# Kernel tuning notes

Hardware: AMD Instinct MI355X
Metric: run time of the kernel (lower is better)

Reference implementation:

```python
import jax, jax.numpy as jnp
import numpy as np
from jax import lax

G = 8  # number of RBF grid points (FastKAN default style)
GRID = jnp.linspace(-2.0, 2.0, G)
DENOM = 4.0 / (G - 1)  # grid spacing used as gaussian width


def _fastkan_conv(x, ln_w, ln_b, Wb, bb, Ws):
    # x: [B, C, H, W]; 3x3 conv, stride 1, pad 1 via patch unfold + FastKAN linear
    B, C, H, W = x.shape
    p = lax.conv_general_dilated_patches(x, (3, 3), (1, 1), ((1, 1), (1, 1)))  # [B, C*9, H, W]
    p = p.transpose(0, 2, 3, 1).reshape(B * H * W, C * 9)  # [N, in]
    # LayerNorm over patch features (FastKAN normalizes before the RBF basis)
    mu = p.mean(-1, keepdims=True)
    var = p.var(-1, keepdims=True)
    pn = (p - mu) / jnp.sqrt(var + 1e-5) * ln_w + ln_b
    # Gaussian RBF basis: [N, in, G]
    rbf = jnp.exp(-jnp.square((pn[:, :, None] - GRID) / DENOM))
    spline = rbf.reshape(B * H * W, -1) @ Ws.T          # [N, out]
    base = jax.nn.silu(p) @ Wb.T + bb                    # [N, out]
    out = spline + base
    return out.reshape(B, H, W, -1).transpose(0, 3, 1, 2)  # [B, out, H, W]


def _bn_relu_pool(h, gamma, beta):
    # BatchNorm2d in training mode (batch stats), ReLU, MaxPool2d(2,2)
    mu = h.mean((0, 2, 3), keepdims=True)
    var = h.var((0, 2, 3), keepdims=True)
    h = (h - mu) / jnp.sqrt(var + 1e-5) * gamma[None, :, None, None] + beta[None, :, None, None]
    h = jax.nn.relu(h)
    return lax.reduce_window(h, -jnp.inf, lax.max, (1, 1, 2, 2), (1, 1, 2, 2), 'VALID')


def setup_inputs() -> dict:
    key = jax.random.key(0)
    ks = jax.random.split(key, 16)
    B, Cin, H, W = 32, 16, 64, 64
    dims = [(Cin * 9, 64), (64 * 9, 128), (128 * 9, 256)]
    inp = {"x": jax.random.normal(ks[0], (B, Cin, H, W), jnp.float32)}
    for i, (fin, fout) in enumerate(dims, 1):
        inp[f"ln_w{i}"] = jnp.ones((fin,), jnp.float32)
        inp[f"ln_b{i}"] = jnp.zeros((fin,), jnp.float32)
        inp[f"Wb{i}"] = jax.random.normal(ks[3 * i], (fout, fin), jnp.float32) * 0.05
        inp[f"bb{i}"] = jnp.zeros((fout,), jnp.float32)
        inp[f"Ws{i}"] = jax.random.normal(ks[3 * i + 1], (fout, fin * G), jnp.float32) * 0.05
        inp[f"g{i}"] = jnp.ones((fout,), jnp.float32)
        inp[f"be{i}"] = jnp.zeros((fout,), jnp.float32)
    return inp


def reference(x, ln_w1, ln_b1, Wb1, bb1, Ws1, g1, be1,
              ln_w2, ln_b2, Wb2, bb2, Ws2, g2, be2,
              ln_w3, ln_b3, Wb3, bb3, Ws3, g3, be3):
    h = _bn_relu_pool(_fastkan_conv(x, ln_w1, ln_b1, Wb1, bb1, Ws1), g1, be1)
    h = _bn_relu_pool(_fastkan_conv(h, ln_w2, ln_b2, Wb2, bb2, Ws2), g2, be2)
    h = _bn_relu_pool(_fastkan_conv(h, ln_w3, ln_b3, Wb3, bb3, Ws3), g3, be3)
    return h.reshape(h.shape[0], -1)  # flatten: [B, 256*8*8]
```

## Files before the change

### kernel.cpp

```cpp
#include <hip/hip_runtime.h>

typedef _Float16 half_t;
typedef __attribute__((ext_vector_type(8))) _Float16 half8;
typedef __attribute__((ext_vector_type(4))) float floatx4;


#define RBF_SCALE 2.1019644f
#define RBF_G0   -4.2039288f
#define RBF_2D    2.40224482f
#define RBF_D2    1.44269504f
#define RBF_Q     0.13533528f

template<int C, int H, int W>
__global__ __launch_bounds__(256)
void ln_prep(const float* __restrict__ x,
             const float* __restrict__ lnw, const float* __restrict__ lnb,
             half_t* __restrict__ pn, half_t* __restrict__ sp)
{
    const int HW = H * W, IN = C * 9;
    const int NL = (IN + 63) / 64;
    const int wv = threadIdx.x >> 6, lane = threadIdx.x & 63;
    const int pix = blockIdx.x * 4 + wv;
    const int b = pix / HW, hw = pix % HW, h = hw / W, w = hw % W;
    const float* xb = x + (long)b * C * HW;

    float v[NL];
    float s = 0.f, s2 = 0.f;
    #pragma unroll
    for (int t = 0; t < NL; ++t) {
        int i = t * 64 + lane;
        float val = 0.f;
        if (i < IN) {
            int ch = i / 9, r = i - ch * 9;
            int y = h + r / 3 - 1, xx = w + r % 3 - 1;
            if (y >= 0 && y < H && xx >= 0 && xx < W)
                val = xb[ch * HW + y * W + xx];
        }
        v[t] = val; s += val; s2 += val * val;
    }
    #pragma unroll
    for (int off = 32; off > 0; off >>= 1) {
        s  += __shfl_down(s,  off, 64);
        s2 += __shfl_down(s2, off, 64);
    }
    s = __shfl(s, 0, 64); s2 = __shfl(s2, 0, 64);
    float mean = s / IN;
    float istd = rsqrtf(s2 / IN - mean * mean + 1e-5f);

    #pragma unroll
    for (int t = 0; t < NL; ++t) {
        int i = t * 64 + lane;
        if (i < IN) {
            float val = v[t];
            float pnv = (val - mean) * istd * lnw[i] + lnb[i];
            pnv = fminf(12.f, fmaxf(-12.f, pnv * RBF_SCALE));
            pn[(long)pix * IN + i] = (half_t)pnv;
            sp[(long)pix * IN + i] = (half_t)(val / (1.f + __expf(-val)));
        }
    }
}

template<int IN, int OUT>
__global__ __launch_bounds__(256)
void conv_w(const float* __restrict__ Ws, const float* __restrict__ Wb,
            half_t* __restrict__ Wt)
{
    const int NIB = (IN + 63) / 64, NSTEP = NIB * 9;
    int idx = blockIdx.x * 256 + threadIdx.x;
    if (idx >= OUT * NSTEP * 64) return;
    int uu = idx & 63;
    int t = idx >> 6;
    int o = t % OUT;
    int s = t / OUT;
    int iblk = s / 9, j = s % 9;
    int ulin = (((uu >> 3) ^ (o & 7)) << 3) + (uu & 7);
    int i = iblk * 64 + ulin;
    float v = 0.f;
    if (i < IN)
        v = (j < 8) ? Ws[(long)o * IN * 8 + i * 8 + j] : Wb[(long)o * IN + i];
    Wt[idx] = (half_t)v;
}

template<int IN, int OUT, int HW, int NB, int SPLIT>
__global__ __launch_bounds__(256)
void kan_gemm(const half_t* __restrict__ pn, const half_t* __restrict__ sp,
              const half_t* __restrict__ Wt, float* __restrict__ out)
{
    const int NIB = (IN + 63) / 64;

    __shared__ half_t As[2][64 * 64];
    __shared__ half_t Bs[2][NB * 64 * 64];

    const int tid = threadIdx.x;
    const int row = tid >> 2, q = tid & 3;
    const int pix = blockIdx.x * 64 + row;
    const half_t* pnrow = pn + (long)pix * IN;
    const half_t* sprow = sp + (long)pix * IN;

    const int wv = tid >> 6, lane = tid & 63;
    const int lr = lane & 15, lq = lane >> 4;
    const int u0 = (2 * q) ^ (row & 7);
    const int u1 = (2 * q + 1) ^ (row & 7);
    const int yoff = blockIdx.y * (4 * NB * 16);

    floatx4 acc[NB][4] = {};
    float r[16], u[16];

    const int grpA = (blockIdx.z * NIB) / SPLIT;
    const int grpB = ((blockIdx.z + 1) * NIB) / SPLIT;
    const int s0 = grpA * 9, s1 = grpB * 9;

    int jg = 0, ibg = grpA;

    auto stageB = [&](int it, int buf) {
        const half_t* wsrc = Wt + (long)it * OUT * 64
                              + (long)(yoff + wv * NB * 16) * 64;
        #pragma unroll
        for (int c = 0; c < NB * 2; ++c) {
            __builtin_amdgcn_global_load_lds(
                (const __attribute__((address_space(1))) void*)(wsrc + c * 512 + lane * 8),
                (__attribute__((address_space(3))) void*)(&Bs[buf][wv * NB * 1024 + c * 512]),
                16, 0, 0);
        }
    };

    auto genA = [&](int buf) {
        const int i0 = ibg * 64 + q * 16;
        const bool ok = (i0 < IN);
        if (jg < 8) {
            if (jg == 0) {
                const half_t* pp = pnrow + (ok ? i0 : 0);
                half8 p0 = *(const half8*)pp;
                half8 p1 = *(const half8*)(pp + 8);
                #pragma unroll
                for (int kk = 0; kk < 8; ++kk) {
                    float t0 = (float)p0[kk], t1 = (float)p1[kk];
                    float d0 = t0 - RBF_G0, d1 = t1 - RBF_G0;
                    r[kk]     = ok ? __builtin_amdgcn_exp2f(-(d0 * d0)) : 0.f;
                    u[kk]     = ok ? __builtin_amdgcn_exp2f(fmaf(RBF_2D, d0, -RBF_D2)) : 0.f;
                    r[kk + 8] = ok ? __builtin_amdgcn_exp2f(-(d1 * d1)) : 0.f;
                    u[kk + 8] = ok ? __builtin_amdgcn_exp2f(fmaf(RBF_2D, d1, -RBF_D2)) : 0.f;
                }
            }
            half8 a0, a1;
            #pragma unroll
            for (int kk = 0; kk < 8; ++kk) {
                a0[kk] = (half_t)r[kk];
                a1[kk] = (half_t)r[kk + 8];
            }
            *(half8*)&As[buf][row * 64 + u0 * 8] = a0;
            *(half8*)&As[buf][row * 64 + u1 * 8] = a1;
            if (jg < 7) {
                #pragma unroll
                for (int kk = 0; kk < 16; ++kk) { r[kk] *= u[kk]; u[kk] *= RBF_Q; }
            }
        } else {
            half8 a0 = half8{}, a1 = half8{};
            if (ok) {
                a0 = *(const half8*)(sprow + i0);
                a1 = *(const half8*)(sprow + i0 + 8);
            }
            *(half8*)&As[buf][row * 64 + u0 * 8] = a0;
            *(half8*)&As[buf][row * 64 + u1 * 8] = a1;
        }
        if (++jg == 9) { jg = 0; ++ibg; }
    };

    auto domfma = [&](int buf) {
        __builtin_amdgcn_s_setprio(1);
        #pragma unroll
        for (int ks = 0; ks < 2; ++ks) {
            half8 af[4], bf[NB];
            #pragma unroll
            for (int mf = 0; mf < 4; ++mf) {
                int rr = mf * 16 + lr;
                af[mf] = *(const half8*)&As[buf][rr * 64 + (((ks * 4 + lq) ^ (rr & 7)) * 8)];
            }
            #pragma unroll
            for (int nb = 0; nb < NB; ++nb) {
                int rr = wv * NB * 16 + nb * 16 + lr;
                bf[nb] = *(const half8*)&Bs[buf][rr * 64 + (((ks * 4 + lq) ^ (rr & 7)) * 8)];
            }
            #pragma unroll
            for (int nb = 0; nb < NB; ++nb)
                #pragma unroll
                for (int mf = 0; mf < 4; ++mf)
                    acc[nb][mf] = __builtin_amdgcn_mfma_f32_16x16x32_f16(
                        bf[nb], af[mf], acc[nb][mf], 0, 0, 0);
        }
        __builtin_amdgcn_s_setprio(0);
    };

    stageB(s0, 0);
    genA(0);
    __syncthreads();

    for (int it = s0; it < s1; ++it) {
        const int cur = (it - s0) & 1, nxt = cur ^ 1;
        if (it + 1 < s1) {
            stageB(it + 1, nxt);
            genA(nxt);
        }
        domfma(cur);
        __syncthreads();
    }

    const long zoff = (long)blockIdx.z * ((long)gridDim.x * 64) * OUT;
    #pragma unroll
    for (int nb = 0; nb < NB; ++nb)
    #pragma unroll
    for (int mf = 0; mf < 4; ++mf)
    #pragma unroll
    for (int reg = 0; reg < 4; ++reg) {
        int o  = yoff + wv * NB * 16 + nb * 16 + lq * 4 + reg;
        int p2 = blockIdx.x * 64 + mf * 16 + lr;
        int b2 = p2 / HW, hw2 = p2 % HW;
        out[zoff + ((long)b2 * OUT + o) * HW + hw2] = acc[nb][mf][reg];
    }
}

__launch_bounds__(256)
__global__ void bn_stats(const float* __restrict__ h, const float* __restrict__ bias,
                         int C, int HW, int B, int nz, float* __restrict__ sums)
{
    int c = blockIdx.y;
    float bbc = bias[c];
    long zstride = (long)B * C * HW;
    int total = B * HW;
    float s = 0.f, s2 = 0.f;
    for (int idx = blockIdx.x * 256 + threadIdx.x; idx < total; idx += 256 * gridDim.x) {
        int b = idx / HW, r = idx % HW;
        long base = ((long)b * C + c) * HW + r;
        float v = bbc;
        for (int z = 0; z < nz; ++z) v += h[z * zstride + base];
        s += v; s2 += v * v;
    }
    for (int off = 32; off > 0; off >>= 1) {
        s  += __shfl_down(s,  off, 64);
        s2 += __shfl_down(s2, off, 64);
    }
    __shared__ float rs[4], rs2[4];
    int lane = threadIdx.x & 63, wid = threadIdx.x >> 6;
    if (lane == 0) { rs[wid] = s; rs2[wid] = s2; }
    __syncthreads();
    if (threadIdx.x == 0) {
        atomicAdd(&sums[c],     rs[0] + rs[1] + rs[2] + rs[3]);
        atomicAdd(&sums[C + c], rs2[0] + rs2[1] + rs2[2] + rs2[3]);
    }
}

__launch_bounds__(256)
__global__ void bn_relu_pool(const float* __restrict__ h, const float* __restrict__ sums,
                             const float* __restrict__ bias,
                             const float* __restrict__ gamma, const float* __restrict__ beta,
                             float* __restrict__ out, int B, int C, int H, int W, int nz)
{
    int Ho = H / 2, Wo = W / 2;
    long total = (long)B * C * Ho * Wo;
    long idx = (long)blockIdx.x * 256 + threadIdx.x;
    if (idx >= total) return;
    int pw = idx % Wo; long t = idx / Wo;
    int ph = t % Ho; t /= Ho;
    int c = t % C; int b = (int)(t / C);

    float M = (float)B * H * W;
    float mean = sums[c] / M;
    float var  = sums[C + c] / M - mean * mean;
    float scale = gamma[c] * rsqrtf(var + 1e-5f);
    float shift = beta[c] - mean * scale + bias[c] * scale;

    long zstride = (long)B * C * H * W;
    const float* hp = h + ((long)b * C + c) * H * W;
    float m = 0.f;
    #pragma unroll
    for (int i = 0; i < 2; ++i)
        #pragma unroll
        for (int j = 0; j < 2; ++j) {
            long off = (2 * ph + i) * W + 2 * pw + j;
            float v = 0.f;
            for (int z = 0; z < nz; ++z) v += hp[z * zstride + off];
            v = v * scale + shift;
            m = fmaxf(m, v);
        }
    out[idx] = m;
}

extern "C" void kernel_launch(void* const* d_in, const int* in_sizes, int n_in,
                              void* d_out, int out_size, void* d_ws, size_t ws_size,
                              hipStream_t stream) {
    const float* x     = (const float*)d_in[0];
    const float* ln_w1 = (const float*)d_in[1];  const float* ln_b1 = (const float*)d_in[2];
    const float* Wb1   = (const float*)d_in[3];  const float* bb1   = (const float*)d_in[4];
    const float* Ws1   = (const float*)d_in[5];  const float* g1    = (const float*)d_in[6];
    const float* be1   = (const float*)d_in[7];
    const float* ln_w2 = (const float*)d_in[8];  const float* ln_b2 = (const float*)d_in[9];
    const float* Wb2   = (const float*)d_in[10]; const float* bb2   = (const float*)d_in[11];
    const float* Ws2   = (const float*)d_in[12]; const float* g2    = (const float*)d_in[13];
    const float* be2   = (const float*)d_in[14];
    const float* ln_w3 = (const float*)d_in[15]; const float* ln_b3 = (const float*)d_in[16];
    const float* Wb3   = (const float*)d_in[17]; const float* bb3   = (const float*)d_in[18];
    const float* Ws3   = (const float*)d_in[19]; const float* g3    = (const float*)d_in[20];
    const float* be3   = (const float*)d_in[21];

    const int B = 32;
    char* ws = (char*)d_ws;
    float*  convbuf = (float*)(ws + 0);
    float*  poolbuf = (float*)(ws + 33554432);
    float*  stats1  = (float*)(ws + 41943040);
    float*  stats2  = (float*)(ws + 41945088);
    float*  stats3  = (float*)(ws + 41947136);
    half_t* wt1     = (half_t*)(ws + 41949184);
    half_t* wt2     = (half_t*)(ws + 42170368);
    half_t* wt3     = (half_t*)(ws + 43497472);
    half_t* pnbuf   = (half_t*)(ws + 48805888);
    half_t* spbuf   = (half_t*)(ws + 86554624);

    hipMemsetAsync(stats1, 0, 6144, stream);

    conv_w<144, 64><<<(64 * 27 * 64 + 255) / 256, 256, 0, stream>>>(Ws1, Wb1, wt1);
    conv_w<576, 128><<<(128 * 81 * 64 + 255) / 256, 256, 0, stream>>>(Ws2, Wb2, wt2);
    conv_w<1152, 256><<<(256 * 162 * 64 + 255) / 256, 256, 0, stream>>>(Ws3, Wb3, wt3);

    {
        const int H = 64, W = 64, OUT = 64;
        int npix = B * H * W;
        ln_prep<16, H, W><<<npix / 4, 256, 0, stream>>>(x, ln_w1, ln_b1, pnbuf, spbuf);
        kan_gemm<144, OUT, H * W, 1, 1><<<dim3(npix / 64, 1, 1), 256, 0, stream>>>(
            pnbuf, spbuf, wt1, convbuf);
        bn_stats<<<dim3(64, OUT), 256, 0, stream>>>(convbuf, bb1, OUT, H * W, B, 1, stats1);
        long tot = (long)B * OUT * (H / 2) * (W / 2);
        bn_relu_pool<<<(tot + 255) / 256, 256, 0, stream>>>(
            convbuf, stats1, bb1, g1, be1, poolbuf, B, OUT, H, W, 1);
    }
    {
        const int H = 32, W = 32, OUT = 128;
        int npix = B * H * W;
        ln_prep<64, H, W><<<npix / 4, 256, 0, stream>>>(poolbuf, ln_w2, ln_b2, pnbuf, spbuf);
        kan_gemm<576, OUT, H * W, 2, 2><<<dim3(npix / 64, 1, 2), 256, 0, stream>>>(
            pnbuf, spbuf, wt2, convbuf);
        bn_stats<<<dim3(16, OUT), 256, 0, stream>>>(convbuf, bb2, OUT, H * W, B, 2, stats2);
        long tot = (long)B * OUT * (H / 2) * (W / 2);
        bn_relu_pool<<<(tot + 255) / 256, 256, 0, stream>>>(
            convbuf, stats2, bb2, g2, be2, poolbuf, B, OUT, H, W, 2);
    }
    {
        const int H = 16, W = 16, OUT = 256;
        int npix = B * H * W;
        ln_prep<128, H, W><<<npix / 4, 256, 0, stream>>>(poolbuf, ln_w3, ln_b3, pnbuf, spbuf);
        kan_gemm<1152, OUT, H * W, 2, 4><<<dim3(npix / 64, 2, 4), 256, 0, stream>>>(
            pnbuf, spbuf, wt3, convbuf);
        bn_stats<<<dim3(8, OUT), 256, 0, stream>>>(convbuf, bb3, OUT, H * W, B, 4, stats3);
        long tot = (long)B * OUT * (H / 2) * (W / 2);
        bn_relu_pool<<<(tot + 255) / 256, 256, 0, stream>>>(
            convbuf, stats3, bb3, g3, be3, (float*)d_out, B, OUT, H, W, 4);
    }
}
```

Baseline: 512.5 us.

## Single-buffer LDS tiles in KAN GEMM and prefetch A inputs into registers

Replaces the double-buffered A/B shared-memory tiles with single buffers and two barriers per k-step. This halves LDS use, which may allow more resident blocks per CU. The pn/sp row chunks are now prefetched into registers one stage ahead, and the out-of-range masking is dropped because zero-padded weights cancel those lanes. The cost is that the weight global-to-LDS load and the A generation are no longer overlapped with the MFMA work inside a block, so latency hiding now depends on other resident blocks.

```diff
diff --git a/kernel.cpp b/kernel.cpp
--- a/kernel.cpp
+++ b/kernel.cpp
@@ -88,8 +88,8 @@
 {
     const int NIB = (IN + 63) / 64;
 
-    __shared__ half_t As[2][64 * 64];
-    __shared__ half_t Bs[2][NB * 64 * 64];
+    __shared__ half_t As[64 * 64];
+    __shared__ half_t Bs[NB * 64 * 64];
 
     const int tid = threadIdx.x;
     const int row = tid >> 2, q = tid & 3;
@@ -105,6 +105,7 @@
 
     floatx4 acc[NB][4] = {};
     float r[16], u[16];
+    half8 pf0, pf1;
 
     const int grpA = (blockIdx.z * NIB) / SPLIT;
     const int grpB = ((blockIdx.z + 1) * NIB) / SPLIT;
@@ -112,34 +113,36 @@
 
     int jg = 0, ibg = grpA;
 
-    auto stageB = [&](int it, int buf) {
+    auto ldglob = [&](const half_t* base, int ib, half8& a, half8& b) {
+        int i0 = ib * 64 + q * 16;
+        const half_t* pp = base + ((i0 < IN) ? i0 : 0);
+        a = *(const half8*)pp;
+        b = *(const half8*)(pp + 8);
+    };
+
+    auto stageB = [&](int it) {
         const half_t* wsrc = Wt + (long)it * OUT * 64
                               + (long)(yoff + wv * NB * 16) * 64;
         #pragma unroll
         for (int c = 0; c < NB * 2; ++c) {
             __builtin_amdgcn_global_load_lds(
                 (const __attribute__((address_space(1))) void*)(wsrc + c * 512 + lane * 8),
-                (__attribute__((address_space(3))) void*)(&Bs[buf][wv * NB * 1024 + c * 512]),
+                (__attribute__((address_space(3))) void*)(&Bs[wv * NB * 1024 + c * 512]),
                 16, 0, 0);
         }
     };
 
-    auto genA = [&](int buf) {
-        const int i0 = ibg * 64 + q * 16;
-        const bool ok = (i0 < IN);
+    auto genA = [&]() {
         if (jg < 8) {
             if (jg == 0) {
-                const half_t* pp = pnrow + (ok ? i0 : 0);
-                half8 p0 = *(const half8*)pp;
-                half8 p1 = *(const half8*)(pp + 8);
                 #pragma unroll
                 for (int kk = 0; kk < 8; ++kk) {
-                    float t0 = (float)p0[kk], t1 = (float)p1[kk];
-                    float d0 = t0 - RBF_G0, d1 = t1 - RBF_G0;
-                    r[kk]     = ok ? __builtin_amdgcn_exp2f(-(d0 * d0)) : 0.f;
-                    u[kk]     = ok ? __builtin_amdgcn_exp2f(fmaf(RBF_2D, d0, -RBF_D2)) : 0.f;
-                    r[kk + 8] = ok ? __builtin_amdgcn_exp2f(-(d1 * d1)) : 0.f;
-                    u[kk + 8] = ok ? __builtin_amdgcn_exp2f(fmaf(RBF_2D, d1, -RBF_D2)) : 0.f;
+                    float d0 = (float)pf0[kk] - RBF_G0;
+                    float d1 = (float)pf1[kk] - RBF_G0;
+                    r[kk]     = __builtin_amdgcn_exp2f(-(d0 * d0));
+                    u[kk]     = __builtin_amdgcn_exp2f(fmaf(RBF_2D, d0, -RBF_D2));
+                    r[kk + 8] = __builtin_amdgcn_exp2f(-(d1 * d1));
+                    u[kk + 8] = __builtin_amdgcn_exp2f(fmaf(RBF_2D, d1, -RBF_D2));
                 }
             }
             half8 a0, a1;
@@ -148,25 +151,22 @@
                 a0[kk] = (half_t)r[kk];
                 a1[kk] = (half_t)r[kk + 8];
             }
-            *(half8*)&As[buf][row * 64 + u0 * 8] = a0;
-            *(half8*)&As[buf][row * 64 + u1 * 8] = a1;
+            *(half8*)&As[row * 64 + u0 * 8] = a0;
+            *(half8*)&As[row * 64 + u1 * 8] = a1;
             if (jg < 7) {
                 #pragma unroll
                 for (int kk = 0; kk < 16; ++kk) { r[kk] *= u[kk]; u[kk] *= RBF_Q; }
             }
+            if (jg == 7) ldglob(sprow, ibg, pf0, pf1);
         } else {
-            half8 a0 = half8{}, a1 = half8{};
-            if (ok) {
-                a0 = *(const half8*)(sprow + i0);
-                a1 = *(const half8*)(sprow + i0 + 8);
-            }
-            *(half8*)&As[buf][row * 64 + u0 * 8] = a0;
-            *(half8*)&As[buf][row * 64 + u1 * 8] = a1;
+            *(half8*)&As[row * 64 + u0 * 8] = pf0;
+            *(half8*)&As[row * 64 + u1 * 8] = pf1;
+            ldglob(pnrow, ibg + 1, pf0, pf1);
         }
         if (++jg == 9) { jg = 0; ++ibg; }
     };
 
-    auto domfma = [&](int buf) {
+    auto domfma = [&]() {
         __builtin_amdgcn_s_setprio(1);
         #pragma unroll
         for (int ks = 0; ks < 2; ++ks) {
@@ -174,12 +174,12 @@
             #pragma unroll
             for (int mf = 0; mf < 4; ++mf) {
                 int rr = mf * 16 + lr;
-                af[mf] = *(const half8*)&As[buf][rr * 64 + (((ks * 4 + lq) ^ (rr & 7)) * 8)];
+                af[mf] = *(const half8*)&As[rr * 64 + (((ks * 4 + lq) ^ (rr & 7)) * 8)];
             }
             #pragma unroll
             for (int nb = 0; nb < NB; ++nb) {
                 int rr = wv * NB * 16 + nb * 16 + lr;
-                bf[nb] = *(const half8*)&Bs[buf][rr * 64 + (((ks * 4 + lq) ^ (rr & 7)) * 8)];
+                bf[nb] = *(const half8*)&Bs[rr * 64 + (((ks * 4 + lq) ^ (rr & 7)) * 8)];
             }
             #pragma unroll
             for (int nb = 0; nb < NB; ++nb)
@@ -191,18 +191,14 @@
         __builtin_amdgcn_s_setprio(0);
     };
 
-    stageB(s0, 0);
-    genA(0);
-    __syncthreads();
+    ldglob(pnrow, grpA, pf0, pf1);
 
     for (int it = s0; it < s1; ++it) {
-        const int cur = (it - s0) & 1, nxt = cur ^ 1;
-        if (it + 1 < s1) {
-            stageB(it + 1, nxt);
-            genA(nxt);
-        }
-        domfma(cur);
         __syncthreads();
+        stageB(it);
+        genA();
+        __syncthreads();
+        domfma();
     }
 
     const long zoff = (long)blockIdx.z * ((long)gridDim.x * 64) * OUT;
```

Result: faster. 479.5 us (-6.4%).
